# Optimization experiments

Measured on AMD Instinct MI355X. Metric: run time of the kernel, lower is better.

Reference implementation:

```python
import jax, jax.numpy as jnp
import numpy as np

B, N, D = 16, 512, 256
HEADS = 8
HIDEF = 1024
BLOCK, WINDOW = 32, 64
LEVELS = 5
PYOUT = 128
NCLS, NANCH = 5, 9
NEG = -1e9


def _sinusoidal_pos(n, d):
    # PositionEmbeddingStatic: deterministic sinusoidal table [n, d]
    pos = np.arange(n)[:, None].astype(np.float64)
    i = np.arange(d)[None, :]
    angle = pos / np.power(10000.0, (2 * (i // 2)) / d)
    pe = np.where(i % 2 == 0, np.sin(angle), np.cos(angle))
    return jnp.asarray(pe, jnp.float32)


def _layernorm(x, g, b, eps=1e-5):
    m = x.mean(-1, keepdims=True)
    v = x.var(-1, keepdims=True)
    return (x - m) * jax.lax.rsqrt(v + eps) * g + b


def _bn(x_bcn, g, b, eps=1e-5):
    # BatchNorm1d in training mode: per-channel batch stats over (B, N)
    m = x_bcn.mean((0, 2), keepdims=True)
    v = x_bcn.var((0, 2), keepdims=True)
    return (x_bcn - m) * jax.lax.rsqrt(v + eps) * g[None, :, None] + b[None, :, None]


def _sparse_attention(x, Wqkv, bqkv, Wo, bo):
    # Windowed block-sparse attention: queries in block i attend to key blocks
    # [i-w, i+w] with w = window_size // block_size. Never materializes SxS.
    Bx, Nx, Dx = x.shape
    H, dh = HEADS, Dx // HEADS
    nb, bs = Nx // BLOCK, BLOCK
    w = WINDOW // BLOCK
    qkv = x @ Wqkv + bqkv
    q, k, v = jnp.split(qkv, 3, axis=-1)

    def to_blocks(t):  # [B,N,D] -> [B,H,nb,bs,dh]
        return t.reshape(Bx, nb, bs, H, dh).transpose(0, 3, 1, 2, 4)

    q, k, v = to_blocks(q), to_blocks(k), to_blocks(v)
    offs = list(range(-w, w + 1))
    # roll by -o puts key block (i+o) at query-block position i
    k_band = jnp.concatenate([jnp.roll(k, -o, axis=2) for o in offs], axis=3)
    v_band = jnp.concatenate([jnp.roll(v, -o, axis=2) for o in offs], axis=3)
    blk = jnp.arange(nb)
    valid = jnp.concatenate(
        [jnp.repeat(((blk + o >= 0) & (blk + o < nb))[:, None], bs, axis=1) for o in offs],
        axis=1)  # [nb, (2w+1)*bs]
    scale = 1.0 / jnp.sqrt(jnp.asarray(dh, x.dtype))
    scores = jnp.einsum('bhnqd,bhnkd->bhnqk', q, k_band) * scale
    scores = jnp.where(valid[None, None, :, None, :], scores, NEG)
    p = jax.nn.softmax(scores, axis=-1)
    o = jnp.einsum('bhnqk,bhnkd->bhnqd', p, v_band)
    o = o.transpose(0, 2, 3, 1, 4).reshape(Bx, Nx, Dx)
    return o @ Wo + bo


def setup_inputs():
    key = jax.random.key(0)
    ks = iter(jax.random.split(key, 48))
    g = lambda shape, s=0.02: jax.random.normal(next(ks), shape, jnp.float32) * s
    z = lambda *shape: jnp.zeros(shape, jnp.float32)
    o = lambda *shape: jnp.ones(shape, jnp.float32)
    return {
        'x': jax.random.normal(next(ks), (B, N, D), jnp.float32),
        'patch_W': g((D, D)), 'patch_b': z(D),
        'ln_g': o(D), 'ln_b': z(D),
        'ff_W1': g((D, HIDEF)), 'ff_b1': z(HIDEF),
        'ff_W2': g((HIDEF, D)), 'ff_b2': z(D),
        'Wqkv': g((D, 3 * D)), 'bqkv': z(3 * D),
        'Wo': g((D, D)), 'bo': z(D),
        'bn1_g': o(D), 'bn1_b': z(D),
        'bn2_g': o(D), 'bn2_b': z(D),
        'pyr_W': g((LEVELS, D, PYOUT)), 'pyr_b': z(LEVELS, PYOUT),
        'fcl_W': g((LEVELS * PYOUT * N, 128), 0.005), 'fcl_b': z(128),
        'addbn_g': o(128), 'addbn_b': z(128),
        'cls_W1': g((128, 256)), 'cls_b1': z(256),
        'cls_W2': g((256, NCLS * NANCH)), 'cls_b2': z(NCLS * NANCH),
        'box_W1': g((128, 128)), 'box_b1': z(128),
        'box_W2': g((128, 4 * NANCH)), 'box_b2': z(4 * NANCH),
    }


def reference(x, patch_W, patch_b, ln_g, ln_b, ff_W1, ff_b1, ff_W2, ff_b2,
              Wqkv, bqkv, Wo, bo, bn1_g, bn1_b, bn2_g, bn2_b,
              pyr_W, pyr_b, fcl_W, fcl_b, addbn_g, addbn_b,
              cls_W1, cls_b1, cls_W2, cls_b2, box_W1, box_b1, box_W2, box_b2):
    pos = _sinusoidal_pos(N, D)

    def ff(h):
        return jax.nn.gelu(h @ ff_W1 + ff_b1) @ ff_W2 + ff_b2

    def mnt(h):
        h = _layernorm(h @ patch_W + patch_b, ln_g, ln_b)  # patch embed + norm
        h = h + pos[None]
        idt = h
        h = ff(h)
        h = _sparse_attention(h, Wqkv, bqkv, Wo, bo)
        h = h + idt
        h = _bn(h.transpose(0, 2, 1), bn1_g, bn1_b).transpose(0, 2, 1)
        idt = h
        h = ff(h) + idt
        h = _bn(h.transpose(0, 2, 1), bn2_g, bn2_b).transpose(0, 2, 1)
        return h

    outs = []
    for _ in range(5):
        x = mnt(x)
        outs.append(x.transpose(0, 2, 1))  # [B, D, N]

    # pyramid: per-level 1x1 conv D -> 128
    feats = [jnp.einsum('bdn,dc->bcn', outs[i], pyr_W[i]) + pyr_b[i][None, :, None]
             for i in range(LEVELS)]
    flat = jnp.concatenate([f.reshape(f.shape[0], -1) for f in feats], axis=1)
    add = (flat @ fcl_W + fcl_b)[:, :, None]          # [B,128,1]
    add = _bn(add, addbn_g, addbn_b).transpose(0, 2, 1)  # [B,1,128]
    cls = jax.nn.relu(add @ cls_W1 + cls_b1) @ cls_W2 + cls_b2
    cls = jax.nn.softmax(cls, axis=-1).reshape(-1, NANCH, NCLS)  # eval mode softmax
    box = (jax.nn.relu(add @ box_W1 + box_b1) @ box_W2 + box_b2).reshape(-1, NANCH, 4)
    return jnp.concatenate([cls, box], axis=-1)  # [B, NANCH, NCLS+4]
```

## Files before the change

### kernel.cpp

```cpp
#include <hip/hip_runtime.h>
#include <hip/hip_bf16.h>
#include <math.h>

#define B_ 16
#define N_ 512
#define D_ 256
#define HEADS_ 8
#define DH_ 32
#define HIDEF_ 1024
#define NBLK_ 16
#define BS_ 32
#define LEVELS_ 5
#define PYOUT_ 128
#define ROWS_ (B_ * N_)
#define FCL_K 327680
#define FCL_KB 256
#define FCL_CHUNKS 1280

typedef __attribute__((ext_vector_type(8))) short short8;
typedef __attribute__((ext_vector_type(4))) short short4v;
typedef __attribute__((ext_vector_type(4))) unsigned short ushort4v;
typedef __attribute__((ext_vector_type(4))) float f32x4;

__device__ __forceinline__ float bf2f(short u) {
    return __uint_as_float(((unsigned int)(unsigned short)u) << 16);
}
__device__ __forceinline__ unsigned short f2bf(float x) {
    __hip_bfloat16 h = __float2bfloat16(x);
    return *reinterpret_cast<unsigned short*>(&h);
}

__device__ __forceinline__ float gelu_f(float x) {
    float x3 = x * x * x;
    return 0.5f * x * (1.f + tanhf(0.7978845608028654f * (x + 0.044715f * x3)));
}

__global__ __launch_bounds__(256) void prep_kernel(
    const float* __restrict__ patch_W, const float* __restrict__ Wqkv,
    const float* __restrict__ Wo, const float* __restrict__ ff_W1,
    const float* __restrict__ ff_W2, const float* __restrict__ pyr_W,
    const float* __restrict__ x_in,
    __hip_bfloat16* __restrict__ patchWt, __hip_bfloat16* __restrict__ qkvWt,
    __hip_bfloat16* __restrict__ WoWt, __hip_bfloat16* __restrict__ W1t,
    __hip_bfloat16* __restrict__ W2t, __hip_bfloat16* __restrict__ pyrWt,
    float* __restrict__ pos, __hip_bfloat16* __restrict__ Xb) {
    __shared__ float tt[32][33];
    int bid = blockIdx.x, t = threadIdx.x;
    if (bid >= 1504) {
        int base = (bid - 1504) * 2048 + t * 8;
        float4 a = *(const float4*)&x_in[base];
        float4 b = *(const float4*)&x_in[base + 4];
        ushort4v u0 = {f2bf(a.x), f2bf(a.y), f2bf(a.z), f2bf(a.w)};
        ushort4v u1 = {f2bf(b.x), f2bf(b.y), f2bf(b.z), f2bf(b.w)};
        *(ushort4v*)((short*)Xb + base) = u0;
        *(ushort4v*)((short*)Xb + base + 4) = u1;
        return;
    }
    if (bid >= 992) {
        int idx = (bid - 992) * 256 + t;
        int n = idx >> 8, i = idx & 255;
        double angle = (double)n / pow(10000.0, (double)(2 * (i >> 1)) / 256.0);
        pos[idx] = (float)((i & 1) ? cos(angle) : sin(angle));
        return;
    }
    const float* W; __hip_bfloat16* Wt; int K, N, bx, by;
    if (bid < 64)       { W = patch_W; Wt = patchWt; K = 256; N = 256; bx = bid % 8; by = bid / 8; }
    else if (bid < 256) { int l = bid - 64;  W = Wqkv;  Wt = qkvWt; K = 256; N = 768;  bx = l % 24; by = l / 24; }
    else if (bid < 320) { int l = bid - 256; W = Wo;    Wt = WoWt;  K = 256; N = 256;  bx = l % 8;  by = l / 8; }
    else if (bid < 576) { int l = bid - 320; W = ff_W1; Wt = W1t;   K = 256; N = 1024; bx = l % 32; by = l / 32; }
    else if (bid < 832) { int l = bid - 576; W = ff_W2; Wt = W2t;   K = 1024; N = 256; bx = l % 8;  by = l / 8; }
    else                { int l = bid - 832; int z = l / 32; int r = l % 32;
                          W = pyr_W + (size_t)z * 256 * 128; Wt = pyrWt + (size_t)z * 256 * 128;
                          K = 256; N = 128; bx = r % 4; by = r / 4; }
    int bx32 = bx * 32, by32 = by * 32;
    int tx = t & 31, ty = t >> 5;
#pragma unroll
    for (int i = 0; i < 32; i += 8)
        tt[ty + i][tx] = W[(size_t)(by32 + ty + i) * N + bx32 + tx];
    __syncthreads();
#pragma unroll
    for (int i = 0; i < 32; i += 8)
        Wt[(size_t)(bx32 + ty + i) * K + by32 + tx] = __float2bfloat16(tt[tx][ty + i]);
}

template <int ACT, bool OUTF, bool OUTB, bool SCAT, bool STATS, int BM, int BN>
__global__ __launch_bounds__(256) void bgemm_kernel(
    const __hip_bfloat16* __restrict__ A, const __hip_bfloat16* __restrict__ Wt,
    const float* __restrict__ bias, const float* __restrict__ resid,
    float* __restrict__ C, __hip_bfloat16* __restrict__ Cb, int M, int Nn, int K,
    int level, float* __restrict__ bnp) {
    __shared__ __hip_bfloat16 Alds[2][BM * 64];
    __shared__ __hip_bfloat16 Blds[2][BN * 64];
    constexpr int WM_ = (BM == 128 && BN == 64) ? 4 : 2;
    constexpr int WN_ = 4 / WM_;
    constexpr int WH = BM / WM_;
    constexpr int WC = BN / WN_;
    constexpr int MW = WH / 16;
    constexpr int NW = WC / 16;
    constexpr int AR = BM / 32;
    constexpr int BR = BN / 32;
    int tid = threadIdx.x;
    int wid = tid >> 6, lane = tid & 63;
    int row0 = blockIdx.y * BM, col0 = blockIdx.x * BN;
    int wr = wid / WN_, wc = wid % WN_;
    int r16 = lane & 15, kq = lane >> 4;

    f32x4 acc[MW][NW];
#pragma unroll
    for (int m = 0; m < MW; m++)
#pragma unroll
        for (int n = 0; n < NW; n++) acc[m][n] = (f32x4){0.f, 0.f, 0.f, 0.f};

    auto stage = [&](int b, int k0) {
#pragma unroll
        for (int i = 0; i < AR; i++) {
            int slot = i * 256 + tid;
            int row = slot >> 3, qp = slot & 7;
            int q = qp ^ ((row >> 1) & 7);
            const __hip_bfloat16* ga = A + (size_t)(row0 + row) * K + k0 + q * 8;
            __builtin_amdgcn_global_load_lds(
                (const __attribute__((address_space(1))) void*)ga,
                (__attribute__((address_space(3))) void*)((char*)&Alds[b][0] + i * 4096 + wid * 1024),
                16, 0, 0);
        }
#pragma unroll
        for (int i = 0; i < BR; i++) {
            int slot = i * 256 + tid;
            int row = slot >> 3, qp = slot & 7;
            int q = qp ^ ((row >> 1) & 7);
            const __hip_bfloat16* gb = Wt + (size_t)(col0 + row) * K + k0 + q * 8;
            __builtin_amdgcn_global_load_lds(
                (const __attribute__((address_space(1))) void*)gb,
                (__attribute__((address_space(3))) void*)((char*)&Blds[b][0] + i * 4096 + wid * 1024),
                16, 0, 0);
        }
    };

    stage(0, 0);
    __syncthreads();
    int cur = 0;
    for (int k0 = 0; k0 < K; k0 += 64) {
        if (k0 + 64 < K) stage(cur ^ 1, k0 + 64);
#pragma unroll
        for (int h = 0; h < 2; h++) {
            short8 af[MW], bf4[NW];
#pragma unroll
            for (int m = 0; m < MW; m++) {
                int row = wr * WH + m * 16 + r16;
                int phys = (h * 4 + kq) ^ ((row >> 1) & 7);
                af[m] = *reinterpret_cast<const short8*>(
                    reinterpret_cast<const char*>(&Alds[cur][0]) + row * 128 + phys * 16);
            }
#pragma unroll
            for (int n = 0; n < NW; n++) {
                int row = wc * WC + n * 16 + r16;
                int phys = (h * 4 + kq) ^ ((row >> 1) & 7);
                bf4[n] = *reinterpret_cast<const short8*>(
                    reinterpret_cast<const char*>(&Blds[cur][0]) + row * 128 + phys * 16);
            }
#pragma unroll
            for (int m = 0; m < MW; m++)
#pragma unroll
                for (int n = 0; n < NW; n++)
                    acc[m][n] = __builtin_amdgcn_mfma_f32_16x16x32_bf16(af[m], bf4[n], acc[m][n], 0, 0, 0);
        }
        __syncthreads();
        cur ^= 1;
    }

    int rg = lane >> 4;
    float s1a[NW], s2a[NW];
#pragma unroll
    for (int n = 0; n < NW; n++) { s1a[n] = 0.f; s2a[n] = 0.f; }
    if (SCAT) {
#pragma unroll
        for (int n = 0; n < NW; n++) {
            int cc = col0 + wc * WC + n * 16 + r16;
            int bb = cc >> 9, nn = cc & 511;
            float* dst = C + (size_t)bb * (LEVELS_ * PYOUT_ * N_) +
                         (size_t)level * PYOUT_ * N_ + nn;
#pragma unroll
            for (int m = 0; m < MW; m++) {
                int rbase = row0 + wr * WH + m * 16 + rg * 4;
#pragma unroll
                for (int j = 0; j < 4; j++) {
                    int ch = rbase + j;
                    dst[(size_t)ch * N_] = acc[m][n][j] + bias[ch];
                }
            }
        }
    } else {
#pragma unroll
        for (int n = 0; n < NW; n++) {
            int cc = col0 + wc * WC + n * 16 + r16;
            float bv = bias[cc];
#pragma unroll
            for (int m = 0; m < MW; m++) {
                int rb = row0 + wr * WH + m * 16 + rg * 4;
#pragma unroll
                for (int j = 0; j < 4; j++) {
                    int r = rb + j;
                    float v = acc[m][n][j] + bv;
                    if (resid) v += resid[(size_t)r * Nn + cc];
                    if (ACT == 1) v = gelu_f(v);
                    if (OUTF) C[(size_t)r * Nn + cc] = v;
                    if (OUTB) Cb[(size_t)r * Nn + cc] = __float2bfloat16(v);
                    if (STATS) { s1a[n] += v; s2a[n] += v * v; }
                }
            }
        }
    }
    if (STATS) {
        float* sc = (float*)&Alds[0][0];
        int part = wid * 4 + rg;
#pragma unroll
        for (int n = 0; n < NW; n++) {
            int c = wc * WC + n * 16 + r16;
            sc[c * 16 + part] = s1a[n];
            sc[BN * 16 + c * 16 + part] = s2a[n];
        }
        __syncthreads();
        if (tid < BN) {
            float a = 0.f, b2 = 0.f;
#pragma unroll
            for (int p = 0; p < 16; p++) {
                a += sc[tid * 16 + p];
                b2 += sc[BN * 16 + tid * 16 + p];
            }
            bnp[blockIdx.y * 256 + col0 + tid] = a;
            bnp[32768 + blockIdx.y * 256 + col0 + tid] = b2;
        }
    }
}

__global__ __launch_bounds__(256) void patchln_kernel(
    const __hip_bfloat16* __restrict__ A, const __hip_bfloat16* __restrict__ Wt,
    const float* __restrict__ bias, const float* __restrict__ lng,
    const float* __restrict__ lnb, const float* __restrict__ pos,
    float* __restrict__ H, __hip_bfloat16* __restrict__ Hb) {
    __shared__ char __attribute__((aligned(16))) smem[73728];
    float (*Cls)[260] = (float(*)[260])smem;
    int tid = threadIdx.x;
    int wid = tid >> 6, lane = tid & 63;
    int row0 = blockIdx.x * 32;
    int r16 = lane & 15, kq = lane >> 4, g = lane >> 4;

    f32x4 acc[2][4];
#pragma unroll
    for (int m = 0; m < 2; m++)
#pragma unroll
        for (int n = 0; n < 4; n++) acc[m][n] = (f32x4){0.f, 0.f, 0.f, 0.f};

    auto stage = [&](int b, int k0) {
        {
            int row = tid >> 3, qp = tid & 7;
            int q = qp ^ ((row >> 1) & 7);
            const __hip_bfloat16* ga = A + (size_t)(row0 + row) * 256 + k0 + q * 8;
            __builtin_amdgcn_global_load_lds(
                (const __attribute__((address_space(1))) void*)ga,
                (__attribute__((address_space(3))) void*)(smem + b * 4096 + wid * 1024),
                16, 0, 0);
        }
#pragma unroll
        for (int i = 0; i < 8; i++) {
            int slot = i * 256 + tid;
            int row = slot >> 3, qp = slot & 7;
            int q = qp ^ ((row >> 1) & 7);
            const __hip_bfloat16* gb = Wt + (size_t)row * 256 + k0 + q * 8;
            __builtin_amdgcn_global_load_lds(
                (const __attribute__((address_space(1))) void*)gb,
                (__attribute__((address_space(3))) void*)(smem + 8192 + b * 32768 + i * 4096 + wid * 1024),
                16, 0, 0);
        }
    };

    stage(0, 0);
    __syncthreads();
    int cur = 0;
    for (int k0 = 0; k0 < 256; k0 += 64) {
        if (k0 + 64 < 256) stage(cur ^ 1, k0 + 64);
        const char* Ab = smem + cur * 4096;
        const char* Bb = smem + 8192 + cur * 32768;
#pragma unroll
        for (int h = 0; h < 2; h++) {
            short8 af[2], bf4[4];
#pragma unroll
            for (int m = 0; m < 2; m++) {
                int row = m * 16 + r16;
                int phys = (h * 4 + kq) ^ ((row >> 1) & 7);
                af[m] = *reinterpret_cast<const short8*>(Ab + row * 128 + phys * 16);
            }
#pragma unroll
            for (int n = 0; n < 4; n++) {
                int row = wid * 64 + n * 16 + r16;
                int phys = (h * 4 + kq) ^ ((row >> 1) & 7);
                bf4[n] = *reinterpret_cast<const short8*>(Bb + row * 128 + phys * 16);
            }
#pragma unroll
            for (int m = 0; m < 2; m++)
#pragma unroll
                for (int n = 0; n < 4; n++)
                    acc[m][n] = __builtin_amdgcn_mfma_f32_16x16x32_bf16(af[m], bf4[n], acc[m][n], 0, 0, 0);
        }
        __syncthreads();
        cur ^= 1;
    }
#pragma unroll
    for (int n = 0; n < 4; n++) {
        int col = wid * 64 + n * 16 + r16;
        float bv = bias[col];
#pragma unroll
        for (int m = 0; m < 2; m++)
#pragma unroll
            for (int j = 0; j < 4; j++)
                Cls[m * 16 + g * 4 + j][col] = acc[m][n][j] + bv;
    }
    __syncthreads();
    float4 g4 = ((const float4*)lng)[lane];
    float4 b4 = ((const float4*)lnb)[lane];
#pragma unroll
    for (int rr = 0; rr < 8; rr++) {
        int r = wid * 8 + rr;
        float4 v = *(const float4*)&Cls[r][lane * 4];
        float s = v.x + v.y + v.z + v.w;
#pragma unroll
        for (int mk = 32; mk; mk >>= 1) s += __shfl_xor(s, mk);
        float mean = s * (1.f / 256.f);
        float dx = v.x - mean, dy = v.y - mean, dz = v.z - mean, dw = v.w - mean;
        float q = dx * dx + dy * dy + dz * dz + dw * dw;
#pragma unroll
        for (int mk = 32; mk; mk >>= 1) q += __shfl_xor(q, mk);
        float rstd = rsqrtf(q * (1.f / 256.f) + 1e-5f);
        int grow = row0 + r;
        float4 p4 = ((const float4*)pos)[(size_t)(grow & (N_ - 1)) * 64 + lane];
        float o0 = dx * rstd * g4.x + b4.x + p4.x;
        float o1 = dy * rstd * g4.y + b4.y + p4.y;
        float o2 = dz * rstd * g4.z + b4.z + p4.z;
        float o3 = dw * rstd * g4.w + b4.w + p4.w;
        ((float4*)(H + (size_t)grow * D_))[lane] = (float4){o0, o1, o2, o3};
        ushort4v u = {f2bf(o0), f2bf(o1), f2bf(o2), f2bf(o3)};
        *((ushort4v*)(Hb + (size_t)grow * D_) + lane) = u;
    }
}

__global__ __launch_bounds__(256) void bn_applyfin_kernel(
    const float* __restrict__ x, const float* __restrict__ bnp, int prows,
    const float* __restrict__ g, const float* __restrict__ b,
    float* __restrict__ y, __hip_bfloat16* __restrict__ yb) {
    int tid = threadIdx.x;
    __shared__ float sm[256], sv[256];
    {
        float s = 0.f, s2 = 0.f;
#pragma unroll 4
        for (int yy = 0; yy < prows; yy++) {
            s += bnp[yy * 256 + tid];
            s2 += bnp[32768 + yy * 256 + tid];
        }
        float m = s * (1.f / 8192.f);
        sm[tid] = m;
        sv[tid] = rsqrtf(s2 * (1.f / 8192.f) - m * m + 1e-5f);
    }
    __syncthreads();
    int lane = tid & 63, w = tid >> 6;
    int row0 = blockIdx.x * 32;
    float4 m4 = *(const float4*)&sm[lane * 4];
    float4 r4 = *(const float4*)&sv[lane * 4];
    float4 g4 = ((const float4*)g)[lane];
    float4 b4 = ((const float4*)b)[lane];
#pragma unroll
    for (int rr = 0; rr < 8; rr++) {
        int row = row0 + w * 8 + rr;
        float4 x4 = ((const float4*)(x + (size_t)row * D_))[lane];
        float o0 = (x4.x - m4.x) * r4.x * g4.x + b4.x;
        float o1 = (x4.y - m4.y) * r4.y * g4.y + b4.y;
        float o2 = (x4.z - m4.z) * r4.z * g4.z + b4.z;
        float o3 = (x4.w - m4.w) * r4.w * g4.w + b4.w;
        if (y) ((float4*)(y + (size_t)row * D_))[lane] = (float4){o0, o1, o2, o3};
        if (yb) {
            ushort4v u = {f2bf(o0), f2bf(o1), f2bf(o2), f2bf(o3)};
            *((ushort4v*)(yb + (size_t)row * D_) + lane) = u;
        }
    }
}

__global__ __launch_bounds__(256) void attn_kernel(
    const __hip_bfloat16* __restrict__ qkv, __hip_bfloat16* __restrict__ outb) {
    int bx = blockIdx.x, h = blockIdx.y, b = blockIdx.z;
    int tid = threadIdx.x;
    int wid = tid >> 6, lane = tid & 63;
    __shared__ __hip_bfloat16 Klds[256 * 32];
    __shared__ __hip_bfloat16 Vt[32 * 264];
    const short* q16 = (const short*)qkv;

#pragma unroll
    for (int r = 0; r < 4; r++) {
        int slot = r * 256 + tid;
        int row = slot >> 2, qp = slot & 3;
        int ql = qp ^ ((row >> 1) & 3);
        int jb = bx * 4 - 2 + (row >> 5);
        jb = jb < 0 ? 0 : (jb > 15 ? 15 : jb);
        const short* ga = q16 + ((size_t)(b * N_ + jb * 32 + (row & 31))) * 768 + 256 + h * 32 + ql * 8;
        __builtin_amdgcn_global_load_lds(
            (const __attribute__((address_space(1))) void*)ga,
            (__attribute__((address_space(3))) void*)((char*)Klds + r * 4096 + wid * 1024),
            16, 0, 0);
    }
    {
        int row = tid;
        int jb = bx * 4 - 2 + (row >> 5);
        jb = jb < 0 ? 0 : (jb > 15 ? 15 : jb);
        const short* gv = q16 + ((size_t)(b * N_ + jb * 32 + (row & 31))) * 768 + 512 + h * 32;
        short8 v0 = *(const short8*)(gv);
        short8 v1 = *(const short8*)(gv + 8);
        short8 v2 = *(const short8*)(gv + 16);
        short8 v3 = *(const short8*)(gv + 24);
        short* vt = (short*)Vt;
#pragma unroll
        for (int e = 0; e < 8; e++) {
            vt[(e) * 264 + row] = v0[e];
            vt[(8 + e) * 264 + row] = v1[e];
            vt[(16 + e) * 264 + row] = v2[e];
            vt[(24 + e) * 264 + row] = v3[e];
        }
    }
    __syncthreads();

    int i = bx * 4 + wid;
    int c = lane & 15, g = lane >> 4;
    const float scale = 0.17677669529663687f;

#pragma unroll
    for (int qt = 0; qt < 2; qt++) {
        const short* qa = q16 + ((size_t)(b * N_ + i * 32 + qt * 16 + c)) * 768 + h * 32 + g * 8;
        short8 bq = *(const short8*)qa;
        f32x4 st[10];
#pragma unroll
        for (int t = 0; t < 10; t++) {
            int jb = i - 2 + (t >> 1);
            if (jb >= 0 && jb < NBLK_) {
                int row = wid * 32 + t * 16 + c;
                int phys = g ^ ((row >> 1) & 3);
                short8 ak = *(const short8*)((const char*)Klds + row * 64 + phys * 16);
                st[t] = __builtin_amdgcn_mfma_f32_16x16x32_bf16(
                    ak, bq, (f32x4){0.f, 0.f, 0.f, 0.f}, 0, 0, 0);
            }
        }
        float mx = -1e30f;
#pragma unroll
        for (int t = 0; t < 10; t++) {
            int jb = i - 2 + (t >> 1);
            if (jb >= 0 && jb < NBLK_) {
#pragma unroll
                for (int j = 0; j < 4; j++) {
                    st[t][j] *= scale;
                    mx = fmaxf(mx, st[t][j]);
                }
            }
        }
        mx = fmaxf(mx, __shfl_xor(mx, 16));
        mx = fmaxf(mx, __shfl_xor(mx, 32));
        float sum = 0.f;
#pragma unroll
        for (int t = 0; t < 10; t++) {
            int jb = i - 2 + (t >> 1);
            if (jb >= 0 && jb < NBLK_) {
#pragma unroll
                for (int j = 0; j < 4; j++) {
                    float e = __expf(st[t][j] - mx);
                    st[t][j] = e;
                    sum += e;
                }
            }
        }
        sum += __shfl_xor(sum, 16);
        sum += __shfl_xor(sum, 32);
        float inv = 1.f / sum;
        f32x4 o0 = (f32x4){0.f, 0.f, 0.f, 0.f};
        f32x4 o1 = (f32x4){0.f, 0.f, 0.f, 0.f};
        const short* vt = (const short*)Vt;
#pragma unroll
        for (int t = 0; t < 10; t++) {
            int jb = i - 2 + (t >> 1);
            if (jb >= 0 && jb < NBLK_) {
                short8 pa = (short8)0;
#pragma unroll
                for (int j = 0; j < 4; j++) pa[j] = (short)f2bf(st[t][j] * inv);
                int kb = wid * 32 + t * 16 + g * 4;
                short4v vb0 = *(const short4v*)(vt + (0 * 16 + c) * 264 + kb);
                short4v vb1 = *(const short4v*)(vt + (1 * 16 + c) * 264 + kb);
                short8 b0 = (short8)0, b1 = (short8)0;
#pragma unroll
                for (int e = 0; e < 4; e++) { b0[e] = vb0[e]; b1[e] = vb1[e]; }
                o0 = __builtin_amdgcn_mfma_f32_16x16x32_bf16(pa, b0, o0, 0, 0, 0);
                o1 = __builtin_amdgcn_mfma_f32_16x16x32_bf16(pa, b1, o1, 0, 0, 0);
            }
        }
#pragma unroll
        for (int j = 0; j < 4; j++) {
            size_t rbase = ((size_t)(b * N_ + i * 32 + qt * 16 + g * 4 + j)) * D_ + h * DH_;
            outb[rbase + c] = __float2bfloat16(o0[j]);
            outb[rbase + 16 + c] = __float2bfloat16(o1[j]);
        }
    }
}

__global__ __launch_bounds__(256) void fcl_partial_kernel(
    const float* __restrict__ flat, const float* __restrict__ W,
    float* __restrict__ partial) {
    int chunk = blockIdx.x;
    int t = threadIdx.x;
    int k0 = chunk * FCL_KB;
    __shared__ float fl[FCL_KB][20];
#pragma unroll
    for (int b = 0; b < 16; b++)
        fl[t][b] = flat[(size_t)b * FCL_K + k0 + t];
    __syncthreads();
    int j = t & 127, bg = t >> 7;
    f32x4 a0 = (f32x4){0.f, 0.f, 0.f, 0.f};
    f32x4 a1 = (f32x4){0.f, 0.f, 0.f, 0.f};
#pragma unroll 8
    for (int k = 0; k < FCL_KB; k++) {
        float w = W[(size_t)(k0 + k) * 128 + j];
        f32x4 f0 = *(const f32x4*)&fl[k][bg * 8];
        f32x4 f1 = *(const f32x4*)&fl[k][bg * 8 + 4];
        a0 += f0 * w;
        a1 += f1 * w;
    }
#pragma unroll
    for (int bi = 0; bi < 4; bi++) {
        partial[((size_t)chunk * 16 + bg * 8 + bi) * 128 + j] = a0[bi];
        partial[((size_t)chunk * 16 + bg * 8 + 4 + bi) * 128 + j] = a1[bi];
    }
}

__global__ __launch_bounds__(256) void fcl_reduce_kernel(
    const float* __restrict__ partial, const float* __restrict__ fcl_b,
    float* __restrict__ add) {
    int c0 = blockIdx.x * 32;
    int t = threadIdx.x;
    int ry = t >> 5, cx = t & 31;
    float s = 0.f;
    for (int r = ry; r < FCL_CHUNKS; r += 8)
        s += partial[(size_t)r * 2048 + c0 + cx];
    __shared__ float red[8][32];
    red[ry][cx] = s; __syncthreads();
    if (ry == 0) {
        float tot = 0.f;
#pragma unroll
        for (int q = 0; q < 8; q++) tot += red[q][cx];
        int col = c0 + cx;
        add[col] = tot + fcl_b[col & 127];
    }
}

__global__ __launch_bounds__(256) void head_kernel(
    const float* __restrict__ add, const float* __restrict__ abg, const float* __restrict__ abb,
    const float* __restrict__ cls_W1, const float* __restrict__ cls_b1,
    const float* __restrict__ cls_W2, const float* __restrict__ cls_b2,
    const float* __restrict__ box_W1, const float* __restrict__ box_b1,
    const float* __restrict__ box_W2, const float* __restrict__ box_b2,
    float* __restrict__ out) {
    __shared__ float a2[16][128];
    __shared__ float cm[16][256];
    __shared__ float cls[16][45];
    __shared__ float bmid[16][128];
    __shared__ float smden[16];
    int t = threadIdx.x;
    if (t < 128) {
        float m = 0.f;
#pragma unroll
        for (int b = 0; b < 16; b++) m += add[b * 128 + t];
        m *= (1.f / 16.f);
        float v = 0.f;
#pragma unroll
        for (int b = 0; b < 16; b++) { float d = add[b * 128 + t] - m; v += d * d; }
        v *= (1.f / 16.f);
        float sc = rsqrtf(v + 1e-5f) * abg[t];
#pragma unroll
        for (int b = 0; b < 16; b++) a2[b][t] = (add[b * 128 + t] - m) * sc + abb[t];
    }
    __syncthreads();
    for (int idx = t; idx < 4096; idx += 256) {
        int m = idx >> 8, c = idx & 255;
        float a = cls_b1[c];
        for (int k = 0; k < 128; k++) a += a2[m][k] * cls_W1[k * 256 + c];
        cm[m][c] = fmaxf(a, 0.f);
    }
    for (int idx = t; idx < 2048; idx += 256) {
        int m = idx >> 7, c = idx & 127;
        float a = box_b1[c];
        for (int k = 0; k < 128; k++) a += a2[m][k] * box_W1[k * 128 + c];
        bmid[m][c] = fmaxf(a, 0.f);
    }
    __syncthreads();
    for (int idx = t; idx < 720; idx += 256) {
        int m = idx / 45, c = idx % 45;
        float a = cls_b2[c];
        for (int k = 0; k < 256; k++) a += cm[m][k] * cls_W2[k * 45 + c];
        cls[m][c] = a;
    }
    __syncthreads();
    if (t < 16) {
        float mx = -1e30f;
        for (int c = 0; c < 45; c++) mx = fmaxf(mx, cls[t][c]);
        float s = 0.f;
        for (int c = 0; c < 45; c++) { float e = expf(cls[t][c] - mx); cls[t][c] = e; s += e; }
        smden[t] = s;
    }
    for (int idx = t; idx < 576; idx += 256) {
        int m = idx / 36, c = idx % 36;
        float a = box_b2[c];
        for (int k = 0; k < 128; k++) a += bmid[m][k] * box_W2[k * 36 + c];
        out[m * 81 + (c >> 2) * 9 + 5 + (c & 3)] = a;
    }
    __syncthreads();
    for (int idx = t; idx < 720; idx += 256) {
        int m = idx / 45, c = idx % 45;
        out[m * 81 + (c / 5) * 9 + (c % 5)] = cls[m][c] / smden[m];
    }
}

extern "C" void kernel_launch(void* const* d_in, const int* in_sizes, int n_in,
                              void* d_out, int out_size, void* d_ws, size_t ws_size,
                              hipStream_t stream) {
    const float* x_in    = (const float*)d_in[0];
    const float* patch_W = (const float*)d_in[1];
    const float* patch_b = (const float*)d_in[2];
    const float* ln_g    = (const float*)d_in[3];
    const float* ln_b    = (const float*)d_in[4];
    const float* ff_W1   = (const float*)d_in[5];
    const float* ff_b1   = (const float*)d_in[6];
    const float* ff_W2   = (const float*)d_in[7];
    const float* ff_b2   = (const float*)d_in[8];
    const float* Wqkv    = (const float*)d_in[9];
    const float* bqkv    = (const float*)d_in[10];
    const float* Wo      = (const float*)d_in[11];
    const float* bo      = (const float*)d_in[12];
    const float* bn1_g   = (const float*)d_in[13];
    const float* bn1_b   = (const float*)d_in[14];
    const float* bn2_g   = (const float*)d_in[15];
    const float* bn2_b   = (const float*)d_in[16];
    const float* pyr_W   = (const float*)d_in[17];
    const float* pyr_b   = (const float*)d_in[18];
    const float* fcl_W   = (const float*)d_in[19];
    const float* fcl_b   = (const float*)d_in[20];
    const float* addbn_g = (const float*)d_in[21];
    const float* addbn_b = (const float*)d_in[22];
    const float* cls_W1  = (const float*)d_in[23];
    const float* cls_b1  = (const float*)d_in[24];
    const float* cls_W2  = (const float*)d_in[25];
    const float* cls_b2  = (const float*)d_in[26];
    const float* box_W1  = (const float*)d_in[27];
    const float* box_b1  = (const float*)d_in[28];
    const float* box_W2  = (const float*)d_in[29];
    const float* box_b2  = (const float*)d_in[30];
    float* out = (float*)d_out;

    float* ws = (float*)d_ws;
    size_t off = 0;
    float* POS   = ws + off; off += 131072;
    float* H     = ws + off; off += 2097152;
    float* T     = ws + off; off += 2097152;
    float* UNION = ws + off; off += 4194304;
    float* FLAT  = ws + off; off += 5242880;
    float* PART  = ws + off; off += (size_t)FCL_CHUNKS * 2048;
    float* BNP   = ws + off; off += 2 * 32768;
    float* ADD   = ws + off; off += 2048;
    __hip_bfloat16* Hb   = (__hip_bfloat16*)(ws + off); off += 1048576;
    __hip_bfloat16* Tb   = (__hip_bfloat16*)(ws + off); off += 1048576;
    __hip_bfloat16* Xb   = (__hip_bfloat16*)(ws + off); off += 1048576;
    __hip_bfloat16* ATb  = (__hip_bfloat16*)(ws + off); off += 1048576;
    __hip_bfloat16* patchWt = (__hip_bfloat16*)(ws + off); off += 32768;
    __hip_bfloat16* qkvWt   = (__hip_bfloat16*)(ws + off); off += 98304;
    __hip_bfloat16* WoWt    = (__hip_bfloat16*)(ws + off); off += 32768;
    __hip_bfloat16* W1t     = (__hip_bfloat16*)(ws + off); off += 131072;
    __hip_bfloat16* W2t     = (__hip_bfloat16*)(ws + off); off += 131072;
    __hip_bfloat16* pyrWt   = (__hip_bfloat16*)(ws + off); off += 81920;
    __hip_bfloat16* MIDb = (__hip_bfloat16*)UNION;
    __hip_bfloat16* QKVb = (__hip_bfloat16*)UNION;

    prep_kernel<<<2528, 256, 0, stream>>>(
        patch_W, Wqkv, Wo, ff_W1, ff_W2, pyr_W, x_in,
        patchWt, qkvWt, WoWt, W1t, W2t, pyrWt, POS, Xb);

    for (int it = 0; it < 5; it++) {
        patchln_kernel<<<256, 256, 0, stream>>>(Xb, patchWt, patch_b, ln_g, ln_b, POS, H, Hb);
        bgemm_kernel<1, false, true, false, false, 128, 128><<<dim3(8, 64), 256, 0, stream>>>(
            Hb, W1t, ff_b1, nullptr, nullptr, MIDb, ROWS_, HIDEF_, D_, 0, nullptr);
        bgemm_kernel<0, false, true, false, false, 64, 64><<<dim3(4, 128), 256, 0, stream>>>(
            MIDb, W2t, ff_b2, nullptr, nullptr, Tb, ROWS_, D_, HIDEF_, 0, nullptr);
        bgemm_kernel<0, false, true, false, false, 128, 64><<<dim3(12, 64), 256, 0, stream>>>(
            Tb, qkvWt, bqkv, nullptr, nullptr, QKVb, ROWS_, 768, D_, 0, nullptr);
        attn_kernel<<<dim3(4, HEADS_, B_), 256, 0, stream>>>(QKVb, ATb);
        bgemm_kernel<0, true, false, false, true, 64, 64><<<dim3(4, 128), 256, 0, stream>>>(
            ATb, WoWt, bo, H, T, nullptr, ROWS_, D_, D_, 0, BNP);
        bn_applyfin_kernel<<<256, 256, 0, stream>>>(T, BNP, 128, bn1_g, bn1_b, H, Hb);
        bgemm_kernel<1, false, true, false, false, 128, 128><<<dim3(8, 64), 256, 0, stream>>>(
            Hb, W1t, ff_b1, nullptr, nullptr, MIDb, ROWS_, HIDEF_, D_, 0, nullptr);
        bgemm_kernel<0, true, false, false, true, 64, 64><<<dim3(4, 128), 256, 0, stream>>>(
            MIDb, W2t, ff_b2, H, T, nullptr, ROWS_, D_, HIDEF_, 0, BNP);
        bn_applyfin_kernel<<<256, 256, 0, stream>>>(T, BNP, 128, bn2_g, bn2_b, nullptr, Xb);
        bgemm_kernel<0, false, false, true, false, 64, 64><<<dim3(128, 2), 256, 0, stream>>>(
            pyrWt + (size_t)it * D_ * PYOUT_, Xb, pyr_b + it * PYOUT_, nullptr,
            FLAT, nullptr, PYOUT_, ROWS_, D_, it, nullptr);
    }

    fcl_partial_kernel<<<FCL_CHUNKS, 256, 0, stream>>>(FLAT, fcl_W, PART);
    fcl_reduce_kernel<<<64, 256, 0, stream>>>(PART, fcl_b, ADD);
    head_kernel<<<1, 256, 0, stream>>>(ADD, addbn_g, addbn_b,
        cls_W1, cls_b1, cls_W2, cls_b2, box_W1, box_b1, box_W2, box_b2, out);
    (void)in_sizes; (void)n_in; (void)out_size; (void)ws_size;
}
```

Baseline: 916.4 us.

## Fuse BN2 apply, pyramid conv and next-iteration patch+LN into one kernel

Adds a bnpatch kernel that applies BN2 to the FF2 output, keeps the normalized bf16 tile in LDS, and from that tile runs both the per-level pyramid 1x1 conv (writing FLAT) and the next iteration's patch GEMM with LayerNorm and positional add. This replaces three kernel launches per iteration and the Xb round trip through global memory. The pyramid path no longer needs the SCAT variant of the GEMM, so that branch is removed. The GEMM also remaps workgroup IDs across groups of eight, which is meant to improve cache locality. In exchange, each block redundantly reduces the 128-row BN partials and uses a large LDS footprint, which may lower occupancy.

```diff
diff --git a/kernel.cpp b/kernel.cpp
--- a/kernel.cpp
+++ b/kernel.cpp
@@ -83,12 +83,12 @@
         Wt[(size_t)(bx32 + ty + i) * K + by32 + tx] = __float2bfloat16(tt[tx][ty + i]);
 }
 
-template <int ACT, bool OUTF, bool OUTB, bool SCAT, bool STATS, int BM, int BN>
+template <int ACT, bool OUTF, bool OUTB, bool STATS, int BM, int BN>
 __global__ __launch_bounds__(256) void bgemm_kernel(
     const __hip_bfloat16* __restrict__ A, const __hip_bfloat16* __restrict__ Wt,
     const float* __restrict__ bias, const float* __restrict__ resid,
     float* __restrict__ C, __hip_bfloat16* __restrict__ Cb, int M, int Nn, int K,
-    int level, float* __restrict__ bnp) {
+    float* __restrict__ bnp) {
     __shared__ __hip_bfloat16 Alds[2][BM * 64];
     __shared__ __hip_bfloat16 Blds[2][BN * 64];
     constexpr int WM_ = (BM == 128 && BN == 64) ? 4 : 2;
@@ -101,7 +101,11 @@
     constexpr int BR = BN / 32;
     int tid = threadIdx.x;
     int wid = tid >> 6, lane = tid & 63;
-    int row0 = blockIdx.y * BM, col0 = blockIdx.x * BN;
+    int flat = blockIdx.y * gridDim.x + blockIdx.x;
+    int q8 = (gridDim.x * gridDim.y) >> 3;
+    int wg = (flat & 7) * q8 + (flat >> 3);
+    int bx = wg % gridDim.x, by = wg / gridDim.x;
+    int row0 = by * BM, col0 = bx * BN;
     int wr = wid / WN_, wc = wid % WN_;
     int r16 = lane & 15, kq = lane >> 4;
 
@@ -172,41 +176,22 @@
     float s1a[NW], s2a[NW];
 #pragma unroll
     for (int n = 0; n < NW; n++) { s1a[n] = 0.f; s2a[n] = 0.f; }
-    if (SCAT) {
-#pragma unroll
-        for (int n = 0; n < NW; n++) {
-            int cc = col0 + wc * WC + n * 16 + r16;
-            int bb = cc >> 9, nn = cc & 511;
-            float* dst = C + (size_t)bb * (LEVELS_ * PYOUT_ * N_) +
-                         (size_t)level * PYOUT_ * N_ + nn;
-#pragma unroll
-            for (int m = 0; m < MW; m++) {
-                int rbase = row0 + wr * WH + m * 16 + rg * 4;
-#pragma unroll
-                for (int j = 0; j < 4; j++) {
-                    int ch = rbase + j;
-                    dst[(size_t)ch * N_] = acc[m][n][j] + bias[ch];
-                }
-            }
-        }
-    } else {
-#pragma unroll
-        for (int n = 0; n < NW; n++) {
-            int cc = col0 + wc * WC + n * 16 + r16;
-            float bv = bias[cc];
-#pragma unroll
-            for (int m = 0; m < MW; m++) {
-                int rb = row0 + wr * WH + m * 16 + rg * 4;
-#pragma unroll
-                for (int j = 0; j < 4; j++) {
-                    int r = rb + j;
-                    float v = acc[m][n][j] + bv;
-                    if (resid) v += resid[(size_t)r * Nn + cc];
-                    if (ACT == 1) v = gelu_f(v);
-                    if (OUTF) C[(size_t)r * Nn + cc] = v;
-                    if (OUTB) Cb[(size_t)r * Nn + cc] = __float2bfloat16(v);
-                    if (STATS) { s1a[n] += v; s2a[n] += v * v; }
-                }
+#pragma unroll
+    for (int n = 0; n < NW; n++) {
+        int cc = col0 + wc * WC + n * 16 + r16;
+        float bv = bias[cc];
+#pragma unroll
+        for (int m = 0; m < MW; m++) {
+            int rb = row0 + wr * WH + m * 16 + rg * 4;
+#pragma unroll
+            for (int j = 0; j < 4; j++) {
+                int r = rb + j;
+                float v = acc[m][n][j] + bv;
+                if (resid) v += resid[(size_t)r * Nn + cc];
+                if (ACT == 1) v = gelu_f(v);
+                if (OUTF) C[(size_t)r * Nn + cc] = v;
+                if (OUTB) Cb[(size_t)r * Nn + cc] = __float2bfloat16(v);
+                if (STATS) { s1a[n] += v; s2a[n] += v * v; }
             }
         }
     }
@@ -227,8 +212,8 @@
                 a += sc[tid * 16 + p];
                 b2 += sc[BN * 16 + tid * 16 + p];
             }
-            bnp[blockIdx.y * 256 + col0 + tid] = a;
-            bnp[32768 + blockIdx.y * 256 + col0 + tid] = b2;
+            bnp[by * 256 + col0 + tid] = a;
+            bnp[32768 + by * 256 + col0 + tid] = b2;
         }
     }
 }
@@ -340,6 +325,187 @@
         ((float4*)(H + (size_t)grow * D_))[lane] = (float4){o0, o1, o2, o3};
         ushort4v u = {f2bf(o0), f2bf(o1), f2bf(o2), f2bf(o3)};
         *((ushort4v*)(Hb + (size_t)grow * D_) + lane) = u;
+    }
+}
+
+template <bool DO_PATCH>
+__global__ __launch_bounds__(256) void bnpatch_kernel(
+    const float* __restrict__ T, const float* __restrict__ bnp,
+    const float* __restrict__ bng, const float* __restrict__ bnb,
+    const __hip_bfloat16* __restrict__ patchWt, const float* __restrict__ patch_b,
+    const float* __restrict__ lng, const float* __restrict__ lnb,
+    const float* __restrict__ pos,
+    const __hip_bfloat16* __restrict__ pyrWt_l, const float* __restrict__ pyr_b_l,
+    int level, float* __restrict__ FLAT,
+    float* __restrict__ H, __hip_bfloat16* __restrict__ Hb) {
+    __shared__ char __attribute__((aligned(16))) smem[68096];
+    float* sm = (float*)(smem + 66048);
+    float* sv = sm + 256;
+    int tid = threadIdx.x;
+    int wid = tid >> 6, lane = tid & 63;
+    int row0 = blockIdx.x * 32;
+    int r16 = lane & 15, kq = lane >> 4, g = lane >> 4;
+    int wr = wid >> 1, wc = wid & 1;
+
+    {
+        float s = 0.f, s2 = 0.f;
+#pragma unroll 4
+        for (int yy = 0; yy < 128; yy++) {
+            s += bnp[yy * 256 + tid];
+            s2 += bnp[32768 + yy * 256 + tid];
+        }
+        float m = s * (1.f / 8192.f);
+        sm[tid] = m;
+        sv[tid] = rsqrtf(s2 * (1.f / 8192.f) - m * m + 1e-5f);
+    }
+    __syncthreads();
+    {
+        float4 m4 = ((const float4*)sm)[lane];
+        float4 r4 = ((const float4*)sv)[lane];
+        float4 g4 = ((const float4*)bng)[lane];
+        float4 b4 = ((const float4*)bnb)[lane];
+#pragma unroll
+        for (int rr = 0; rr < 8; rr++) {
+            int r = wid * 8 + rr;
+            float4 x4 = ((const float4*)(T + (size_t)(row0 + r) * D_))[lane];
+            float o0 = (x4.x - m4.x) * r4.x * g4.x + b4.x;
+            float o1 = (x4.y - m4.y) * r4.y * g4.y + b4.y;
+            float o2 = (x4.z - m4.z) * r4.z * g4.z + b4.z;
+            float o3 = (x4.w - m4.w) * r4.w * g4.w + b4.w;
+            ushort4v u = {f2bf(o0), f2bf(o1), f2bf(o2), f2bf(o3)};
+            int c = lane >> 1;
+            int phys = c ^ (r & 7);
+            *(ushort4v*)(smem + r * 512 + phys * 16 + (lane & 1) * 8) = u;
+        }
+    }
+    __syncthreads();
+
+    if (DO_PATCH) {
+        f32x4 acc[8];
+#pragma unroll
+        for (int n = 0; n < 8; n++) acc[n] = (f32x4){0.f, 0.f, 0.f, 0.f};
+        for (int k0 = 0; k0 < 256; k0 += 64) {
+#pragma unroll
+            for (int i = 0; i < 8; i++) {
+                int slot = i * 256 + tid;
+                int row = slot >> 3, qp = slot & 7;
+                int q = qp ^ ((row >> 1) & 7);
+                const __hip_bfloat16* gb = patchWt + (size_t)row * 256 + k0 + q * 8;
+                __builtin_amdgcn_global_load_lds(
+                    (const __attribute__((address_space(1))) void*)gb,
+                    (__attribute__((address_space(3))) void*)(smem + 16384 + i * 4096 + wid * 1024),
+                    16, 0, 0);
+            }
+            __syncthreads();
+#pragma unroll
+            for (int h = 0; h < 2; h++) {
+                int arow = wr * 16 + r16;
+                int ac = (k0 >> 3) + h * 4 + kq;
+                int aphys = ac ^ (arow & 7);
+                short8 af = *(const short8*)(smem + arow * 512 + aphys * 16);
+                short8 bf4[8];
+#pragma unroll
+                for (int n = 0; n < 8; n++) {
+                    int brow = wc * 128 + n * 16 + r16;
+                    int bphys = (h * 4 + kq) ^ ((brow >> 1) & 7);
+                    bf4[n] = *(const short8*)(smem + 16384 + brow * 128 + bphys * 16);
+                }
+#pragma unroll
+                for (int n = 0; n < 8; n++)
+                    acc[n] = __builtin_amdgcn_mfma_f32_16x16x32_bf16(af, bf4[n], acc[n], 0, 0, 0);
+            }
+            __syncthreads();
+        }
+        float (*Cls)[260] = (float(*)[260])(smem + 16384);
+#pragma unroll
+        for (int n = 0; n < 8; n++) {
+            int col = wc * 128 + n * 16 + r16;
+            float bv = patch_b[col];
+#pragma unroll
+            for (int j = 0; j < 4; j++)
+                Cls[wr * 16 + g * 4 + j][col] = acc[n][j] + bv;
+        }
+        __syncthreads();
+        float4 g4 = ((const float4*)lng)[lane];
+        float4 b4 = ((const float4*)lnb)[lane];
+#pragma unroll
+        for (int rr = 0; rr < 8; rr++) {
+            int r = wid * 8 + rr;
+            float4 v = *(const float4*)&Cls[r][lane * 4];
+            float s = v.x + v.y + v.z + v.w;
+#pragma unroll
+            for (int mk = 32; mk; mk >>= 1) s += __shfl_xor(s, mk);
+            float mean = s * (1.f / 256.f);
+            float dx = v.x - mean, dy = v.y - mean, dz = v.z - mean, dw = v.w - mean;
+            float q = dx * dx + dy * dy + dz * dz + dw * dw;
+#pragma unroll
+            for (int mk = 32; mk; mk >>= 1) q += __shfl_xor(q, mk);
+            float rstd = rsqrtf(q * (1.f / 256.f) + 1e-5f);
+            int grow = row0 + r;
+            float4 p4 = ((const float4*)pos)[(size_t)(grow & (N_ - 1)) * 64 + lane];
+            float o0 = dx * rstd * g4.x + b4.x + p4.x;
+            float o1 = dy * rstd * g4.y + b4.y + p4.y;
+            float o2 = dz * rstd * g4.z + b4.z + p4.z;
+            float o3 = dw * rstd * g4.w + b4.w + p4.w;
+            ((float4*)(H + (size_t)grow * D_))[lane] = (float4){o0, o1, o2, o3};
+            ushort4v u = {f2bf(o0), f2bf(o1), f2bf(o2), f2bf(o3)};
+            *((ushort4v*)(Hb + (size_t)grow * D_) + lane) = u;
+        }
+    }
+
+    f32x4 pacc[4];
+#pragma unroll
+    for (int n = 0; n < 4; n++) pacc[n] = (f32x4){0.f, 0.f, 0.f, 0.f};
+    for (int k0 = 0; k0 < 256; k0 += 64) {
+#pragma unroll
+        for (int i = 0; i < 4; i++) {
+            int slot = i * 256 + tid;
+            int row = slot >> 3, qp = slot & 7;
+            int q = qp ^ ((row >> 1) & 7);
+            const __hip_bfloat16* gb = pyrWt_l + (size_t)row * 256 + k0 + q * 8;
+            __builtin_amdgcn_global_load_lds(
+                (const __attribute__((address_space(1))) void*)gb,
+                (__attribute__((address_space(3))) void*)(smem + 49664 + i * 4096 + wid * 1024),
+                16, 0, 0);
+        }
+        __syncthreads();
+#pragma unroll
+        for (int h = 0; h < 2; h++) {
+            int arow = wr * 16 + r16;
+            int ac = (k0 >> 3) + h * 4 + kq;
+            int aphys = ac ^ (arow & 7);
+            short8 af = *(const short8*)(smem + arow * 512 + aphys * 16);
+            short8 bf4[4];
+#pragma unroll
+            for (int n = 0; n < 4; n++) {
+                int brow = wc * 64 + n * 16 + r16;
+                int bphys = (h * 4 + kq) ^ ((brow >> 1) & 7);
+                bf4[n] = *(const short8*)(smem + 49664 + brow * 128 + bphys * 16);
+            }
+#pragma unroll
+            for (int n = 0; n < 4; n++)
+                pacc[n] = __builtin_amdgcn_mfma_f32_16x16x32_bf16(af, bf4[n], pacc[n], 0, 0, 0);
+        }
+        __syncthreads();
+    }
+    float (*olds)[33] = (float(*)[33])(smem + 16384);
+#pragma unroll
+    for (int n = 0; n < 4; n++) {
+        int ch = wc * 64 + n * 16 + r16;
+        float bv = pyr_b_l[ch];
+#pragma unroll
+        for (int j = 0; j < 4; j++)
+            olds[ch][wr * 16 + g * 4 + j] = pacc[n][j] + bv;
+    }
+    __syncthreads();
+    {
+        int ch = tid >> 1, half = tid & 1;
+        int bb = row0 >> 9, nn0 = (row0 & 511) + half * 16;
+        float* dst = FLAT + (size_t)bb * 327680 + (size_t)(level * 128 + ch) * 512 + nn0;
+        const float* src = &olds[ch][half * 16];
+#pragma unroll
+        for (int q = 0; q < 4; q++)
+            *(float4*)(dst + q * 4) = *(const float4*)(src + q * 4);
     }
 }
 
@@ -683,26 +849,32 @@
         patch_W, Wqkv, Wo, ff_W1, ff_W2, pyr_W, x_in,
         patchWt, qkvWt, WoWt, W1t, W2t, pyrWt, POS, Xb);
 
+    patchln_kernel<<<256, 256, 0, stream>>>(Xb, patchWt, patch_b, ln_g, ln_b, POS, H, Hb);
+
     for (int it = 0; it < 5; it++) {
-        patchln_kernel<<<256, 256, 0, stream>>>(Xb, patchWt, patch_b, ln_g, ln_b, POS, H, Hb);
-        bgemm_kernel<1, false, true, false, false, 128, 128><<<dim3(8, 64), 256, 0, stream>>>(
-            Hb, W1t, ff_b1, nullptr, nullptr, MIDb, ROWS_, HIDEF_, D_, 0, nullptr);
-        bgemm_kernel<0, false, true, false, false, 64, 64><<<dim3(4, 128), 256, 0, stream>>>(
-            MIDb, W2t, ff_b2, nullptr, nullptr, Tb, ROWS_, D_, HIDEF_, 0, nullptr);
-        bgemm_kernel<0, false, true, false, false, 128, 64><<<dim3(12, 64), 256, 0, stream>>>(
-            Tb, qkvWt, bqkv, nullptr, nullptr, QKVb, ROWS_, 768, D_, 0, nullptr);
+        bgemm_kernel<1, false, true, false, 128, 128><<<dim3(8, 64), 256, 0, stream>>>(
+            Hb, W1t, ff_b1, nullptr, nullptr, MIDb, ROWS_, HIDEF_, D_, nullptr);
+        bgemm_kernel<0, false, true, false, 64, 64><<<dim3(4, 128), 256, 0, stream>>>(
+            MIDb, W2t, ff_b2, nullptr, nullptr, Tb, ROWS_, D_, HIDEF_, nullptr);
+        bgemm_kernel<0, false, true, false, 128, 64><<<dim3(12, 64), 256, 0, stream>>>(
+            Tb, qkvWt, bqkv, nullptr, nullptr, QKVb, ROWS_, 768, D_, nullptr);
         attn_kernel<<<dim3(4, HEADS_, B_), 256, 0, stream>>>(QKVb, ATb);
-        bgemm_kernel<0, true, false, false, true, 64, 64><<<dim3(4, 128), 256, 0, stream>>>(
-            ATb, WoWt, bo, H, T, nullptr, ROWS_, D_, D_, 0, BNP);
+        bgemm_kernel<0, true, false, true, 64, 64><<<dim3(4, 128), 256, 0, stream>>>(
+            ATb, WoWt, bo, H, T, nullptr, ROWS_, D_, D_, BNP);
         bn_applyfin_kernel<<<256, 256, 0, stream>>>(T, BNP, 128, bn1_g, bn1_b, H, Hb);
-        bgemm_kernel<1, false, true, false, false, 128, 128><<<dim3(8, 64), 256, 0, stream>>>(
-            Hb, W1t, ff_b1, nullptr, nullptr, MIDb, ROWS_, HIDEF_, D_, 0, nullptr);
-        bgemm_kernel<0, true, false, false, true, 64, 64><<<dim3(4, 128), 256, 0, stream>>>(
-            MIDb, W2t, ff_b2, H, T, nullptr, ROWS_, D_, HIDEF_, 0, BNP);
-        bn_applyfin_kernel<<<256, 256, 0, stream>>>(T, BNP, 128, bn2_g, bn2_b, nullptr, Xb);
-        bgemm_kernel<0, false, false, true, false, 64, 64><<<dim3(128, 2), 256, 0, stream>>>(
-            pyrWt + (size_t)it * D_ * PYOUT_, Xb, pyr_b + it * PYOUT_, nullptr,
-            FLAT, nullptr, PYOUT_, ROWS_, D_, it, nullptr);
+        bgemm_kernel<1, false, true, false, 128, 128><<<dim3(8, 64), 256, 0, stream>>>(
+            Hb, W1t, ff_b1, nullptr, nullptr, MIDb, ROWS_, HIDEF_, D_, nullptr);
+        bgemm_kernel<0, true, false, true, 64, 64><<<dim3(4, 128), 256, 0, stream>>>(
+            MIDb, W2t, ff_b2, H, T, nullptr, ROWS_, D_, HIDEF_, BNP);
+        if (it < 4) {
+            bnpatch_kernel<true><<<256, 256, 0, stream>>>(
+                T, BNP, bn2_g, bn2_b, patchWt, patch_b, ln_g, ln_b, POS,
+                pyrWt + (size_t)it * D_ * PYOUT_, pyr_b + it * PYOUT_, it, FLAT, H, Hb);
+        } else {
+            bnpatch_kernel<false><<<256, 256, 0, stream>>>(
+                T, BNP, bn2_g, bn2_b, patchWt, patch_b, ln_g, ln_b, POS,
+                pyrWt + (size_t)it * D_ * PYOUT_, pyr_b + it * PYOUT_, it, FLAT, H, Hb);
+        }
     }
 
     fcl_partial_kernel<<<FCL_CHUNKS, 256, 0, stream>>>(FLAT, fcl_W, PART);
```

Result: faster. 873.1 us, median of 2 (-4.7%).
